# Kernel optimization log

Hardware: AMD Instinct MI355X
Metric: run time of the kernel (lower is better)

## Reference

```python
import jax, jax.numpy as jnp
import numpy as np

B = 262144
MAXC = 13  # fixed pad size from torch.zeros(13, 3)
CAMERA_HEIGHT = 1.6


def setup_inputs() -> dict:
    key = jax.random.key(0)
    k1, k2, k3, k4 = jax.random.split(key, 4)
    lon = jax.random.uniform(k1, (B, MAXC, 1), jnp.float32, -np.pi, np.pi)
    # up corners: lat strictly negative so y = sin(lat) < 0 and the scale s > 0
    lat = jax.random.uniform(k2, (B, MAXC, 1), jnp.float32, -1.4, -0.2)
    GT_up = jnp.concatenate([lon, lat], axis=-1)  # [B, MAXC, 2]
    corner_nums = 4 + jax.random.randint(k3, (B,), 0, 9)  # in [4, 12]; num+1 <= 13
    up_down_ratio = jax.random.uniform(k4, (B,), jnp.float32, 0.5, 2.0)
    return {"GT_up": GT_up, "corner_nums": corner_nums, "up_down_ratio": up_down_ratio}


def reference(GT_up, corner_nums, up_down_ratio):
    lon = GT_up[..., 0]
    lat = GT_up[..., 1]
    # EquirecTransformer.lonlat2xyz (y is vertical axis)
    x = jnp.cos(lat) * jnp.sin(lon)
    y = jnp.sin(lat)
    z = jnp.cos(lat) * jnp.cos(lon)
    xyz = jnp.stack([x, y, z], axis=-1)  # [B, MAXC, 3]
    # lonlat2xyz_up: scale so vertical coord equals -cH*ratio
    s = -(CAMERA_HEIGHT * up_down_ratio[:, None, None]) / xyz[..., 1:2]
    xyz = xyz * s

    j = jnp.arange(MAXC)                                   # corner index
    nums = corner_nums[:, None]                            # [B, 1]
    valid = j[None, :] < nums                              # [B, MAXC]
    next_idx = jnp.where(j[None, :] + 1 == nums, 0, jnp.minimum(j + 1, MAXC - 1))
    c_next = jnp.take_along_axis(xyz, next_idx[..., None], axis=1)
    vec = c_next - xyz                                     # corners[j+1] - corners[j]
    # mask invalid edges to a safe vector so normalize is finite
    vec = jnp.where(valid[..., None], vec, jnp.array([1.0, 0.0, 0.0], xyz.dtype))
    # cross(vec, (0,1,0)) = (-vz, 0, vx), then L2-normalize
    n = jnp.stack([-vec[..., 2], jnp.zeros_like(vec[..., 0]), vec[..., 0]], axis=-1)
    n = n / jnp.linalg.norm(n, axis=-1, keepdims=True)
    # output: normals for j < num, normal[0] repeated at j == num, zeros after
    out = jnp.where(valid[..., None], n, jnp.zeros_like(n))
    wrap = (j[None, :] == nums)[..., None]                 # [B, MAXC, 1]
    out = jnp.where(wrap, n[:, 0:1, :], out)
    return out  # [B, 13, 3]
```

## Files before the change

### kernel.cpp

```cpp
#include <hip/hip_runtime.h>
#include <math.h>

#define NB 262144
#define MAXC 13
#define INV_2PI 0.15915494309189535f

__global__ __launch_bounds__(256) void render_normals_kernel(
    const float* __restrict__ gt,
    const int* __restrict__ corner_nums,
    const float* __restrict__ ratio,
    float* __restrict__ out)
{
    int t = blockIdx.x * blockDim.x + threadIdx.x;
    if (t >= NB * MAXC) return;
    int b = t / MAXC;
    int j = t - b * MAXC;
    int nums = corner_nums[b];

    float ox = 0.0f, oz = 0.0f;
    if (j <= nums) {
        int i0, i1;
        if (j == nums) { i0 = 0; i1 = 1; }
        else           { i0 = j; i1 = (j + 1 == nums) ? 0 : (j + 1); }

        float hs = -1.6f * ratio[b];
        const float2* g2 = (const float2*)gt;
        float2 p0 = g2[b * MAXC + i0];
        float2 p1 = g2[b * MAXC + i1];

        float a0 = p0.x * INV_2PI, t0 = p0.y * INV_2PI;
        float sl0 = __sinf(p0.x), cl0 = __cosf(p0.x);
        float st0 = __sinf(p0.y), ct0 = __cosf(p0.y);
        float k0 = hs * ct0 * __frcp_rn(st0);
        float x0 = k0 * sl0, z0 = k0 * cl0;
        (void)a0; (void)t0;

        float sl1 = __sinf(p1.x), cl1 = __cosf(p1.x);
        float st1 = __sinf(p1.y), ct1 = __cosf(p1.y);
        float k1 = hs * ct1 * __frcp_rn(st1);
        float x1 = k1 * sl1, z1 = k1 * cl1;

        float dx = x1 - x0;
        float dz = z1 - z0;
        float inv = __frsqrt_rn(dx * dx + dz * dz);
        ox = -dz * inv;
        oz =  dx * inv;
    }

    out[3 * t + 0] = ox;
    out[3 * t + 1] = 0.0f;
    out[3 * t + 2] = oz;
}

extern "C" void kernel_launch(void* const* d_in, const int* in_sizes, int n_in,
                              void* d_out, int out_size, void* d_ws, size_t ws_size,
                              hipStream_t stream) {
    const float* gt     = (const float*)d_in[0];
    const int*   nums   = (const int*)d_in[1];
    const float* ratio  = (const float*)d_in[2];
    float* out = (float*)d_out;

    int total = NB * MAXC;
    int block = 256;
    int grid = (total + block - 1) / block;
    render_normals_kernel<<<grid, block, 0, stream>>>(gt, nums, ratio, out);
}
```

Baseline: 88.13 us.

## Stage per-batch corners in LDS, compute each corner once, vectorize I/O

Each block now handles 64 batches. It loads their corner lon/lat with float4 copies into shared memory, computes each corner's scaled x/z once, and then forms edge normals from shared memory. The output is assembled in shared memory and written back with coalesced float4 stores. This removes the duplicated trig work per edge and the stride-3 scalar stores, at the cost of three block barriers and about 20 KB of LDS per block, which may limit occupancy.

```diff
diff --git a/kernel.cpp b/kernel.cpp
--- a/kernel.cpp
+++ b/kernel.cpp
@@ -3,65 +3,85 @@
 
 #define NB 262144
 #define MAXC 13
-#define INV_2PI 0.15915494309189535f
+#define BPB 64
+#define NTH 256
+#define CORNERS (BPB * MAXC)
+#define GT_FLOATS (BPB * MAXC * 2)
+#define OUT_FLOATS (BPB * MAXC * 3)
 
-__global__ __launch_bounds__(256) void render_normals_kernel(
+__global__ __launch_bounds__(NTH) void render_normals_kernel(
     const float* __restrict__ gt,
     const int* __restrict__ corner_nums,
     const float* __restrict__ ratio,
     float* __restrict__ out)
 {
-    int t = blockIdx.x * blockDim.x + threadIdx.x;
-    if (t >= NB * MAXC) return;
-    int b = t / MAXC;
-    int j = t - b * MAXC;
-    int nums = corner_nums[b];
+    __shared__ __align__(16) float s_buf[OUT_FLOATS];
+    __shared__ float s_x[CORNERS];
+    __shared__ float s_z[CORNERS];
+    __shared__ float s_hs[BPB];
+    __shared__ int   s_nums[BPB];
 
-    float ox = 0.0f, oz = 0.0f;
-    if (j <= nums) {
-        int i0, i1;
-        if (j == nums) { i0 = 0; i1 = 1; }
-        else           { i0 = j; i1 = (j + 1 == nums) ? 0 : (j + 1); }
+    const int tid = threadIdx.x;
+    const int b0  = blockIdx.x * BPB;
 
-        float hs = -1.6f * ratio[b];
-        const float2* g2 = (const float2*)gt;
-        float2 p0 = g2[b * MAXC + i0];
-        float2 p1 = g2[b * MAXC + i1];
+    {
+        const float4* src = (const float4*)(gt + (size_t)b0 * (MAXC * 2));
+        float4* dst = (float4*)s_buf;
+        for (int i = tid; i < GT_FLOATS / 4; i += NTH) dst[i] = src[i];
+    }
+    if (tid < BPB) {
+        s_nums[tid] = corner_nums[b0 + tid];
+        s_hs[tid]   = -1.6f * ratio[b0 + tid];
+    }
+    __syncthreads();
 
-        float a0 = p0.x * INV_2PI, t0 = p0.y * INV_2PI;
-        float sl0 = __sinf(p0.x), cl0 = __cosf(p0.x);
-        float st0 = __sinf(p0.y), ct0 = __cosf(p0.y);
-        float k0 = hs * ct0 * __frcp_rn(st0);
-        float x0 = k0 * sl0, z0 = k0 * cl0;
-        (void)a0; (void)t0;
+    for (int i = tid; i < CORNERS; i += NTH) {
+        float2 p = ((const float2*)s_buf)[i];
+        int b = i / MAXC;
+        float sl = __sinf(p.x), cl = __cosf(p.x);
+        float st = __sinf(p.y), ct = __cosf(p.y);
+        float k = s_hs[b] * ct * __frcp_rn(st);
+        s_x[i] = k * sl;
+        s_z[i] = k * cl;
+    }
+    __syncthreads();
 
-        float sl1 = __sinf(p1.x), cl1 = __cosf(p1.x);
-        float st1 = __sinf(p1.y), ct1 = __cosf(p1.y);
-        float k1 = hs * ct1 * __frcp_rn(st1);
-        float x1 = k1 * sl1, z1 = k1 * cl1;
+    for (int i = tid; i < CORNERS; i += NTH) {
+        int b = i / MAXC;
+        int j = i - b * MAXC;
+        int nums = s_nums[b];
+        float ox = 0.0f, oz = 0.0f;
+        if (j <= nums) {
+            int i0 = (j == nums) ? 0 : j;
+            int i1 = (j == nums) ? 1 : ((j + 1 == nums) ? 0 : j + 1);
+            int base = b * MAXC;
+            float dx = s_x[base + i1] - s_x[base + i0];
+            float dz = s_z[base + i1] - s_z[base + i0];
+            float inv = __frsqrt_rn(dx * dx + dz * dz);
+            ox = -dz * inv;
+            oz =  dx * inv;
+        }
+        s_buf[3 * i + 0] = ox;
+        s_buf[3 * i + 1] = 0.0f;
+        s_buf[3 * i + 2] = oz;
+    }
+    __syncthreads();
 
-        float dx = x1 - x0;
-        float dz = z1 - z0;
-        float inv = __frsqrt_rn(dx * dx + dz * dz);
-        ox = -dz * inv;
-        oz =  dx * inv;
+    {
+        const float4* sv = (const float4*)s_buf;
+        float4* o4 = (float4*)(out + (size_t)b0 * (MAXC * 3));
+        for (int i = tid; i < OUT_FLOATS / 4; i += NTH) o4[i] = sv[i];
     }
-
-    out[3 * t + 0] = ox;
-    out[3 * t + 1] = 0.0f;
-    out[3 * t + 2] = oz;
 }
 
 extern "C" void kernel_launch(void* const* d_in, const int* in_sizes, int n_in,
                               void* d_out, int out_size, void* d_ws, size_t ws_size,
                               hipStream_t stream) {
-    const float* gt     = (const float*)d_in[0];
-    const int*   nums   = (const int*)d_in[1];
-    const float* ratio  = (const float*)d_in[2];
+    const float* gt    = (const float*)d_in[0];
+    const int*   nums  = (const int*)d_in[1];
+    const float* ratio = (const float*)d_in[2];
     float* out = (float*)d_out;
 
-    int total = NB * MAXC;
-    int block = 256;
-    int grid = (total + block - 1) / block;
-    render_normals_kernel<<<grid, block, 0, stream>>>(gt, nums, ratio, out);
+    int grid = NB / BPB;
+    render_normals_kernel<<<grid, NTH, 0, stream>>>(gt, nums, ratio, out);
 }
```

Result: no change. 88.68 us (+0.6%).
